# Performance work log

Hardware: AMD Instinct MI355X
Metric: run time of the kernel (lower is better)

The kernel has to match this reference:

```python
import jax, jax.numpy as jnp
import numpy as np

STEPS = 10
FIRE_RATE = 0.5
INPUT_CHANNELS = 1
EPS = 1e-5
PAD = 4  # (kernel_size-1)//2 for kernel_size=9


def setup_inputs() -> dict:
    key = jax.random.key(0)
    ks = jax.random.split(key, 8)
    B, H, W, C, HID = 4, 192, 192, 16, 128
    x = jax.random.normal(ks[0], (B, H, W, C), dtype=jnp.float32)
    rand_u = jax.random.uniform(ks[1], (STEPS, B, 1, H, W), dtype=jnp.float32)
    w_p0 = jax.random.normal(ks[2], (C, 1, 9, 9), dtype=jnp.float32) * 0.05
    b_p0 = jax.random.normal(ks[3], (C,), dtype=jnp.float32) * 0.05
    w_fc0 = jax.random.normal(ks[4], (HID, 2 * C), dtype=jnp.float32) * (1.0 / np.sqrt(2 * C))
    b_fc0 = jax.random.normal(ks[5], (HID,), dtype=jnp.float32) * 0.05
    w_fc1 = jax.random.normal(ks[6], (C, HID), dtype=jnp.float32) * (1.0 / np.sqrt(HID))
    gamma = jnp.ones((HID,), dtype=jnp.float32)
    beta = jnp.zeros((HID,), dtype=jnp.float32)
    return {"x": x, "rand_u": rand_u, "w_p0": w_p0, "b_p0": b_p0,
            "w_fc0": w_fc0, "b_fc0": b_fc0, "w_fc1": w_fc1,
            "gamma": gamma, "beta": beta}


def _depthwise(x, w, b):
    # x: [B,C,H,W], w: [C,1,9,9] depthwise, reflect padding
    xp = jnp.pad(x, ((0, 0), (0, 0), (PAD, PAD), (PAD, PAD)), mode="reflect")
    y = jax.lax.conv_general_dilated(
        xp, w, window_strides=(1, 1), padding="VALID",
        feature_group_count=x.shape[1],
        dimension_numbers=("NCHW", "OIHW", "NCHW"))
    return y + b[None, :, None, None]


def _nca_forward(x, rand_u, w_p0, b_p0, w_fc0, b_fc0, w_fc1, gamma, beta):
    x = jnp.transpose(x, (0, 3, 1, 2))  # NHWC -> NCHW

    def step(x, u):
        y1 = _depthwise(x, w_p0, b_p0)
        dx = jnp.concatenate((x, y1), axis=1)              # [B,2C,H,W]
        h = jnp.einsum("oc,bchw->bohw", w_fc0, dx) + b_fc0[None, :, None, None]
        # BatchNorm2d with track_running_stats=False: batch stats every step
        mean = jnp.mean(h, axis=(0, 2, 3), keepdims=True)
        var = jnp.mean((h - mean) ** 2, axis=(0, 2, 3), keepdims=True)
        h = gamma[None, :, None, None] * (h - mean) * jax.lax.rsqrt(var + EPS) \
            + beta[None, :, None, None]
        h = jax.nn.relu(h)
        d = jnp.einsum("oc,bchw->bohw", w_fc1, h)          # fc1, no bias
        mask = (u > FIRE_RATE).astype(x.dtype)             # [B,1,H,W]
        x2 = x + d * mask
        # keep the original input channels frozen
        x_new = jnp.concatenate((x[:, :INPUT_CHANNELS], x2[:, INPUT_CHANNELS:]), axis=1)
        return x_new, None

    x, _ = jax.lax.scan(step, x, rand_u)
    return jnp.transpose(x, (0, 2, 3, 1))  # NCHW -> NHWC


def reference(x, rand_u, w_p0, b_p0, w_fc0, b_fc0, w_fc1, gamma, beta):
    return _nca_forward(x, rand_u, w_p0, b_p0, w_fc0, b_fc0, w_fc1, gamma, beta)
```

## Files before the change

### kernel.cpp

```cpp
#include <hip/hip_runtime.h>

constexpr int Bn    = 4;
constexpr int Hn    = 192;
constexpr int Wn    = 192;
constexpr int Cn    = 16;
constexpr int HIDn  = 128;
constexpr int HWn   = Hn * Wn;
constexpr int BHWn  = Bn * HWn;
constexpr int STEPSn = 10;
constexpr int PADn  = 4;
constexpr int KSn   = 9;
constexpr float EPSf  = 1e-5f;
constexpr float FIREf = 0.5f;

constexpr int VY    = 3;
constexpr int SROWS = VY + 8;
constexpr int SCOLS = 72;
constexpr int TPXc  = 64 * VY;
constexpr int CBLK  = BHWn / TPXc;
constexpr int TPIc  = HWn / TPXc;

typedef __attribute__((ext_vector_type(8))) short short8;
typedef __attribute__((ext_vector_type(4))) float f32x4;

static __device__ __forceinline__ unsigned f2bfu(float f) {
    union { float f; unsigned u; } v; v.f = f;
    return (v.u + 0x7FFFu + ((v.u >> 16) & 1u)) >> 16;
}
static __device__ __forceinline__ short f2bf(float f) { return (short)f2bfu(f); }
static __device__ __forceinline__ float bf2f(unsigned short h) {
    union { unsigned u; float f; } v; v.u = ((unsigned)h) << 16;
    return v.f;
}
static __device__ __forceinline__ int refl(int v, int n) {
    v = v < 0 ? -v : v;
    v = v >= n ? 2 * n - 2 - v : v;
    return v;
}

__global__ void k_prep(const float* __restrict__ wp,
                       const float* __restrict__ wfc1,
                       const float* __restrict__ wfc0,
                       float* __restrict__ wtc,
                       float* __restrict__ wt1,
                       short* __restrict__ bfrag)
{
    int tid = threadIdx.x;
    for (int i = tid; i < KSn * KSn * Cn; i += 256) {
        int t = i / Cn, c = i - t * Cn;
        wtc[i] = wp[c * (KSn * KSn) + t];
    }
    for (int i = tid; i < HIDn * Cn; i += 256) {
        int o = i / Cn, c = i - o * Cn;
        wt1[i] = wfc1[c * HIDn + o];
    }
    for (int i = tid; i < 8 * 64 * 8; i += 256) {
        int nt = i >> 9;
        int rem = i & 511;
        int l = rem >> 3, j = rem & 7;
        int n = nt * 16 + (l & 15);
        int k = (l >> 4) * 8 + j;
        bfrag[i] = f2bf(wfc0[n * 32 + k]);
    }
}

#define FMA4(A, Q, V) \
    A.x = fmaf(Q.x, V.x, A.x); A.y = fmaf(Q.y, V.y, A.y); \
    A.z = fmaf(Q.z, V.z, A.z); A.w = fmaf(Q.w, V.w, A.w);

__global__ __launch_bounds__(256) void k_fused(
    const float* __restrict__ xin,
    const float* __restrict__ wtc,
    const float* __restrict__ bp,
    const short* __restrict__ bfrag,
    const float* __restrict__ bfc0,
    unsigned short* __restrict__ hbf,
    float2* __restrict__ part)
{
    __shared__ __align__(16) char smraw[4 * SROWS * SCOLS * 16];
    float4* stg = (float4*)smraw;
    float (*sdx)[33] = (float(*)[33])smraw;
    float2 (*psum)[HIDn] = (float2(*)[HIDn])(smraw + TPXc * 33 * 4);

    int tid  = threadIdx.x;
    int lane = tid & 63;
    int w    = __builtin_amdgcn_readfirstlane(tid >> 6);

    int blk = blockIdx.x;
    int b   = blk / TPIc;
    int t   = blk - b * TPIc;
    int ty  = t / 3;
    int tx  = t - ty * 3;
    int y0  = ty * VY;
    int x0  = tx * 64;

    const float4* xb4 = (const float4*)(xin + (size_t)b * HWn * Cn);
    int rrow[SROWS];
#pragma unroll
    for (int ri = 0; ri < SROWS; ++ri)
        rrow[ri] = refl(y0 + ri - PADn, Hn) * (Wn * 4);

    float4* stw = stg + w * (SROWS * SCOLS);
#pragma unroll
    for (int it = 0; it < 13; ++it) {
        int e = it * 64 + lane;
        if (e < SROWS * SCOLS) {
            int ri  = e / SCOLS;
            int col = e - ri * SCOLS;
            int gc  = refl(x0 + col - PADn, Wn);
            stw[e] = xb4[rrow[ri] + gc * 4 + w];
        }
    }

    const float4* wt4 = (const float4*)wtc;
    float4 bq = ((const float4*)bp)[w];
    float4 a0 = bq, a1 = bq, a2 = bq;
#pragma unroll
    for (int ri = 0; ri < SROWS; ++ri) {
#pragma unroll
        for (int dx = 0; dx < KSn; ++dx) {
            float4 v = stw[ri * SCOLS + lane + dx];
            if (ri <= 8)            { float4 q = wt4[(ri * KSn + dx) * 4 + w];        FMA4(a0, q, v); }
            if (ri >= 1 && ri <= 9) { float4 q = wt4[((ri - 1) * KSn + dx) * 4 + w];  FMA4(a1, q, v); }
            if (ri >= 2)            { float4 q = wt4[((ri - 2) * KSn + dx) * 4 + w];  FMA4(a2, q, v); }
        }
    }
    float4 cen0 = stw[4 * SCOLS + lane + 4];
    float4 cen1 = stw[5 * SCOLS + lane + 4];
    float4 cen2 = stw[6 * SCOLS + lane + 4];

    __syncthreads();

#pragma unroll
    for (int r = 0; r < VY; ++r) {
        int px = r * 64 + lane;
        float4 cv = r == 0 ? cen0 : (r == 1 ? cen1 : cen2);
        float4 av = r == 0 ? a0   : (r == 1 ? a1   : a2);
        sdx[px][4 * w + 0] = cv.x;  sdx[px][4 * w + 1] = cv.y;
        sdx[px][4 * w + 2] = cv.z;  sdx[px][4 * w + 3] = cv.w;
        sdx[px][Cn + 4 * w + 0] = av.x;  sdx[px][Cn + 4 * w + 1] = av.y;
        sdx[px][Cn + 4 * w + 2] = av.z;  sdx[px][Cn + 4 * w + 3] = av.w;
    }
    __syncthreads();

    int l15 = lane & 15;
    int kg  = lane >> 4;

    short8 A[3];
#pragma unroll
    for (int mt = 0; mt < 3; ++mt) {
        int px = 48 * w + mt * 16 + l15;
#pragma unroll
        for (int j = 0; j < 8; ++j)
            A[mt][j] = f2bf(sdx[px][kg * 8 + j]);
    }

    short8 Bf[8];
    const short8* bgp = (const short8*)bfrag;
#pragma unroll
    for (int nt = 0; nt < 8; ++nt) Bf[nt] = bgp[nt * 64 + lane];

#pragma unroll
    for (int nt = 0; nt < 8; ++nt) {
        int o = nt * 16 + l15;
        float bn = bfc0[o];
        float s = 0.f, q = 0.f;
#pragma unroll
        for (int mt = 0; mt < 3; ++mt) {
            f32x4 c = {bn, bn, bn, bn};
            c = __builtin_amdgcn_mfma_f32_16x16x32_bf16(A[mt], Bf[nt], c, 0, 0, 0);
            s += c[0] + c[1] + c[2] + c[3];
            q += c[0]*c[0] + c[1]*c[1] + c[2]*c[2] + c[3]*c[3];
            unsigned lo = (f2bfu(c[1]) << 16) | f2bfu(c[0]);
            unsigned hi = (f2bfu(c[3]) << 16) | f2bfu(c[2]);
            int pxb = 48 * w + 16 * mt + 4 * kg;
            int p   = (y0 + (pxb >> 6)) * Wn + x0 + (pxb & 63);
            *(uint2*)(hbf + (size_t)(b * HIDn + o) * HWn + p) = make_uint2(lo, hi);
        }
        s += __shfl_xor(s, 16, 64);  q += __shfl_xor(q, 16, 64);
        s += __shfl_xor(s, 32, 64);  q += __shfl_xor(q, 32, 64);
        if (kg == 0) psum[w][o] = make_float2(s, q);
    }
    __syncthreads();

    if (tid < HIDn) {
        float2 p0 = psum[0][tid], p1 = psum[1][tid];
        float2 p2 = psum[2][tid], p3 = psum[3][tid];
        part[(size_t)tid * CBLK + blk] =
            make_float2(p0.x + p1.x + p2.x + p3.x, p0.y + p1.y + p2.y + p3.y);
    }
}

__global__ __launch_bounds__(256) void k_combine(
    const float2* __restrict__ part,
    const float* __restrict__ gamma,
    const float* __restrict__ beta,
    float2* __restrict__ scsh)
{
    int o   = blockIdx.x;
    int tid = threadIdx.x;
    float s = 0.f, q = 0.f;
    for (int i = tid; i < CBLK; i += 256) {
        float2 v = part[(size_t)o * CBLK + i];
        s += v.x; q += v.y;
    }
#pragma unroll
    for (int off = 32; off > 0; off >>= 1) {
        s += __shfl_xor(s, off, 64);
        q += __shfl_xor(q, off, 64);
    }
    __shared__ float rs[4], rq[4];
    int wv = tid >> 6;
    if ((tid & 63) == 0) { rs[wv] = s; rq[wv] = q; }
    __syncthreads();
    if (tid == 0) {
        float S = rs[0] + rs[1] + rs[2] + rs[3];
        float Q = rq[0] + rq[1] + rq[2] + rq[3];
        float mean = S * (1.0f / BHWn);
        float var  = Q * (1.0f / BHWn) - mean * mean;
        float g    = gamma[o] * rsqrtf(var + EPSf);
        scsh[o] = make_float2(g, beta[o] - mean * g);
    }
}

__global__ __launch_bounds__(256) void k_update(
    const float* __restrict__ xin,
    const unsigned short* __restrict__ hbf,
    const float2* __restrict__ scsh,
    const float* __restrict__ wt1,
    const float* __restrict__ u,
    float* __restrict__ xout)
{
    __shared__ float pacc[4][64][17];

    int tid  = threadIdx.x;
    int lane = tid & 63;
    int w    = __builtin_amdgcn_readfirstlane(tid >> 6);

    int blk = blockIdx.x;
    int b   = blk / (HWn / 64);
    int pb  = (blk - b * (HWn / 64)) * 64;
    int p   = pb + lane;

    const unsigned short* hsrc = hbf + (size_t)b * HIDn * HWn + p;

    float acc[Cn];
#pragma unroll
    for (int c = 0; c < Cn; ++c) acc[c] = 0.f;

#pragma unroll 4
    for (int j = 0; j < 32; ++j) {
        int o = w * 32 + j;
        float2 g = scsh[o];
        float hv = bf2f(hsrc[(size_t)o * HWn]);
        float hn = fmaxf(fmaf(hv, g.x, g.y), 0.f);
        const float* wr = wt1 + o * Cn;
#pragma unroll
        for (int c = 0; c < Cn; ++c) acc[c] = fmaf(wr[c], hn, acc[c]);
    }

#pragma unroll
    for (int c = 0; c < Cn; ++c) pacc[w][lane][c] = acc[c];
    __syncthreads();

    float4 r = make_float4(0.f, 0.f, 0.f, 0.f);
#pragma unroll
    for (int w2 = 0; w2 < 4; ++w2) {
        r.x += pacc[w2][lane][4 * w + 0];
        r.y += pacc[w2][lane][4 * w + 1];
        r.z += pacc[w2][lane][4 * w + 2];
        r.w += pacc[w2][lane][4 * w + 3];
    }
    if (w == 0) r.x = 0.f;

    float m = u[(size_t)b * HWn + p] > FIREf ? 1.f : 0.f;
    size_t xoff = ((size_t)b * HWn + p) * Cn + 4 * w;
    float4 xv = *(const float4*)(xin + xoff);
    xv.x = fmaf(r.x, m, xv.x);
    xv.y = fmaf(r.y, m, xv.y);
    xv.z = fmaf(r.z, m, xv.z);
    xv.w = fmaf(r.w, m, xv.w);
    *(float4*)(xout + xoff) = xv;
}

extern "C" void kernel_launch(void* const* d_in, const int* in_sizes, int n_in,
                              void* d_out, int out_size, void* d_ws, size_t ws_size,
                              hipStream_t stream) {
    const float* x0   = (const float*)d_in[0];
    const float* ru   = (const float*)d_in[1];
    const float* wp   = (const float*)d_in[2];
    const float* bp   = (const float*)d_in[3];
    const float* wfc0 = (const float*)d_in[4];
    const float* bfc0 = (const float*)d_in[5];
    const float* wfc1 = (const float*)d_in[6];
    const float* gm   = (const float*)d_in[7];
    const float* bt   = (const float*)d_in[8];

    float* ws = (float*)d_ws;
    unsigned short* hbf = (unsigned short*)ws;
    float* xbuf  = ws + 9437184;
    float* wtc   = xbuf + 2359296;
    float* wt1   = wtc + 1312;
    short* bfrag = (short*)(wt1 + 2048);
    float2* part = (float2*)(wt1 + 2048 + 2048);
    float2* scsh = part + (size_t)HIDn * CBLK;

    k_prep<<<1, 256, 0, stream>>>(wp, wfc1, wfc0, wtc, wt1, bfrag);

    const float* xcur = x0;
    for (int s = 0; s < STEPSn; ++s) {
        k_fused<<<CBLK, 256, 0, stream>>>(xcur, wtc, bp, bfrag, bfc0, hbf, part);
        k_combine<<<HIDn, 256, 0, stream>>>(part, gm, bt, scsh);
        float* xo = (s == STEPSn - 1) ? (float*)d_out : xbuf;
        k_update<<<BHWn / 64, 256, 0, stream>>>(xcur, hbf, scsh, wt1,
                                                ru + (size_t)s * BHWn, xo);
        xcur = xo;
    }
}
```

Measured before the change: 448.5 us.

## Use MFMA for fc1, store hidden pixel-major, bf16 staging of conv input

The update kernel now computes fc1 with bf16 MFMA over a pixel-major hidden buffer instead of scalar FMAs over a channel-major one. The fused kernel writes the hidden activations in pixel-major layout, transposes the fc0 MFMA operands, and stages the conv input tile in LDS as bf16. The tile height drops from 3 to 2 rows, with a launch-bounds occupancy hint. This trades extra bf16 rounding of the state and hidden activations for fewer scalar FMAs, less LDS traffic and contiguous hidden loads.

Measured after the change: 592.1 us. 1.32x slower.

```diff
diff --git a/kernel.cpp b/kernel.cpp
--- a/kernel.cpp
+++ b/kernel.cpp
@@ -13,7 +13,7 @@
 constexpr float EPSf  = 1e-5f;
 constexpr float FIREf = 0.5f;
 
-constexpr int VY    = 3;
+constexpr int VY    = 2;
 constexpr int SROWS = VY + 8;
 constexpr int SCOLS = 72;
 constexpr int TPXc  = 64 * VY;
@@ -28,9 +28,11 @@
     return (v.u + 0x7FFFu + ((v.u >> 16) & 1u)) >> 16;
 }
 static __device__ __forceinline__ short f2bf(float f) { return (short)f2bfu(f); }
-static __device__ __forceinline__ float bf2f(unsigned short h) {
-    union { unsigned u; float f; } v; v.u = ((unsigned)h) << 16;
-    return v.f;
+static __device__ __forceinline__ unsigned pk2(float a, float b) {
+    return f2bfu(a) | (f2bfu(b) << 16);
+}
+static __device__ __forceinline__ float asf(unsigned u) {
+    union { unsigned u; float f; } v; v.u = u; return v.f;
 }
 static __device__ __forceinline__ int refl(int v, int n) {
     v = v < 0 ? -v : v;
@@ -42,33 +44,29 @@
                        const float* __restrict__ wfc1,
                        const float* __restrict__ wfc0,
                        float* __restrict__ wtc,
-                       float* __restrict__ wt1,
-                       short* __restrict__ bfrag)
+                       short* __restrict__ bfrag,
+                       short* __restrict__ w1f)
 {
     int tid = threadIdx.x;
     for (int i = tid; i < KSn * KSn * Cn; i += 256) {
         int t = i / Cn, c = i - t * Cn;
         wtc[i] = wp[c * (KSn * KSn) + t];
     }
-    for (int i = tid; i < HIDn * Cn; i += 256) {
-        int o = i / Cn, c = i - o * Cn;
-        wt1[i] = wfc1[c * HIDn + o];
-    }
     for (int i = tid; i < 8 * 64 * 8; i += 256) {
         int nt = i >> 9;
         int rem = i & 511;
         int l = rem >> 3, j = rem & 7;
-        int n = nt * 16 + (l & 15);
-        int k = (l >> 4) * 8 + j;
-        bfrag[i] = f2bf(wfc0[n * 32 + k]);
-    }
-}
-
-#define FMA4(A, Q, V) \
-    A.x = fmaf(Q.x, V.x, A.x); A.y = fmaf(Q.y, V.y, A.y); \
-    A.z = fmaf(Q.z, V.z, A.z); A.w = fmaf(Q.w, V.w, A.w);
-
-__global__ __launch_bounds__(256) void k_fused(
+        bfrag[i] = f2bf(wfc0[(nt * 16 + (l & 15)) * 32 + (l >> 4) * 8 + j]);
+    }
+    for (int i = tid; i < 4 * 64 * 8; i += 256) {
+        int ks = i >> 9;
+        int rem = i & 511;
+        int l = rem >> 3, j = rem & 7;
+        w1f[i] = f2bf(wfc1[(l & 15) * HIDn + ks * 32 + (l >> 4) * 8 + j]);
+    }
+}
+
+__global__ __launch_bounds__(256, 4) void k_fused(
     const float* __restrict__ xin,
     const float* __restrict__ wtc,
     const float* __restrict__ bp,
@@ -77,10 +75,10 @@
     unsigned short* __restrict__ hbf,
     float2* __restrict__ part)
 {
-    __shared__ __align__(16) char smraw[4 * SROWS * SCOLS * 16];
-    float4* stg = (float4*)smraw;
-    float (*sdx)[33] = (float(*)[33])smraw;
-    float2 (*psum)[HIDn] = (float2(*)[HIDn])(smraw + TPXc * 33 * 4);
+    __shared__ __align__(16) char smraw[4 * SROWS * SCOLS * 8];
+    uint2* stg = (uint2*)smraw;
+    unsigned* sdx = (unsigned*)smraw;
+    float2* psum = (float2*)(smraw + TPXc * 20 * 4);
 
     int tid  = threadIdx.x;
     int lane = tid & 63;
@@ -100,92 +98,105 @@
     for (int ri = 0; ri < SROWS; ++ri)
         rrow[ri] = refl(y0 + ri - PADn, Hn) * (Wn * 4);
 
-    float4* stw = stg + w * (SROWS * SCOLS);
-#pragma unroll
-    for (int it = 0; it < 13; ++it) {
+    uint2* stw = stg + w * (SROWS * SCOLS);
+#pragma unroll
+    for (int it = 0; it < 12; ++it) {
         int e = it * 64 + lane;
         if (e < SROWS * SCOLS) {
             int ri  = e / SCOLS;
             int col = e - ri * SCOLS;
             int gc  = refl(x0 + col - PADn, Wn);
-            stw[e] = xb4[rrow[ri] + gc * 4 + w];
+            float4 v = xb4[rrow[ri] + gc * 4 + w];
+            stw[e] = make_uint2(pk2(v.x, v.y), pk2(v.z, v.w));
         }
     }
 
     const float4* wt4 = (const float4*)wtc;
     float4 bq = ((const float4*)bp)[w];
-    float4 a0 = bq, a1 = bq, a2 = bq;
+    float4 a0 = bq, a1 = bq;
+    uint2 cen0, cen1;
 #pragma unroll
     for (int ri = 0; ri < SROWS; ++ri) {
+        uint2 tv[KSn];
+#pragma unroll
+        for (int dx = 0; dx < KSn; ++dx) tv[dx] = stw[ri * SCOLS + lane + dx];
+        if (ri == 4) cen0 = tv[4];
+        if (ri == 5) cen1 = tv[4];
 #pragma unroll
         for (int dx = 0; dx < KSn; ++dx) {
-            float4 v = stw[ri * SCOLS + lane + dx];
-            if (ri <= 8)            { float4 q = wt4[(ri * KSn + dx) * 4 + w];        FMA4(a0, q, v); }
-            if (ri >= 1 && ri <= 9) { float4 q = wt4[((ri - 1) * KSn + dx) * 4 + w];  FMA4(a1, q, v); }
-            if (ri >= 2)            { float4 q = wt4[((ri - 2) * KSn + dx) * 4 + w];  FMA4(a2, q, v); }
+            float c0 = asf(tv[dx].x << 16), c1 = asf(tv[dx].x & 0xffff0000u);
+            float c2 = asf(tv[dx].y << 16), c3 = asf(tv[dx].y & 0xffff0000u);
+            if (ri <= 8) {
+                float4 q = wt4[(ri * KSn + dx) * 4 + w];
+                a0.x = fmaf(q.x, c0, a0.x); a0.y = fmaf(q.y, c1, a0.y);
+                a0.z = fmaf(q.z, c2, a0.z); a0.w = fmaf(q.w, c3, a0.w);
+            }
+            if (ri >= 1) {
+                float4 q = wt4[((ri - 1) * KSn + dx) * 4 + w];
+                a1.x = fmaf(q.x, c0, a1.x); a1.y = fmaf(q.y, c1, a1.y);
+                a1.z = fmaf(q.z, c2, a1.z); a1.w = fmaf(q.w, c3, a1.w);
+            }
         }
     }
-    float4 cen0 = stw[4 * SCOLS + lane + 4];
-    float4 cen1 = stw[5 * SCOLS + lane + 4];
-    float4 cen2 = stw[6 * SCOLS + lane + 4];
-
     __syncthreads();
 
 #pragma unroll
     for (int r = 0; r < VY; ++r) {
         int px = r * 64 + lane;
-        float4 cv = r == 0 ? cen0 : (r == 1 ? cen1 : cen2);
-        float4 av = r == 0 ? a0   : (r == 1 ? a1   : a2);
-        sdx[px][4 * w + 0] = cv.x;  sdx[px][4 * w + 1] = cv.y;
-        sdx[px][4 * w + 2] = cv.z;  sdx[px][4 * w + 3] = cv.w;
-        sdx[px][Cn + 4 * w + 0] = av.x;  sdx[px][Cn + 4 * w + 1] = av.y;
-        sdx[px][Cn + 4 * w + 2] = av.z;  sdx[px][Cn + 4 * w + 3] = av.w;
+        uint2 cv = r ? cen1 : cen0;
+        float4 av = r ? a1 : a0;
+        unsigned* row = sdx + px * 20;
+        *(uint2*)(row + 2 * w)     = cv;
+        *(uint2*)(row + 8 + 2 * w) = make_uint2(pk2(av.x, av.y), pk2(av.z, av.w));
     }
     __syncthreads();
 
     int l15 = lane & 15;
     int kg  = lane >> 4;
 
-    short8 A[3];
-#pragma unroll
-    for (int mt = 0; mt < 3; ++mt) {
-        int px = 48 * w + mt * 16 + l15;
-#pragma unroll
-        for (int j = 0; j < 8; ++j)
-            A[mt][j] = f2bf(sdx[px][kg * 8 + j]);
-    }
-
-    short8 Bf[8];
+    short8 Bd[VY];
+#pragma unroll
+    for (int mt = 0; mt < VY; ++mt) {
+        int px = 32 * w + 16 * mt + l15;
+        Bd[mt] = *(const short8*)(sdx + px * 20 + kg * 4);
+    }
+    short8 Af[8];
     const short8* bgp = (const short8*)bfrag;
 #pragma unroll
-    for (int nt = 0; nt < 8; ++nt) Bf[nt] = bgp[nt * 64 + lane];
-
+    for (int nt = 0; nt < 8; ++nt) Af[nt] = bgp[nt * 64 + lane];
+
+    unsigned short* hb = hbf + (size_t)b * HWn * HIDn;
 #pragma unroll
     for (int nt = 0; nt < 8; ++nt) {
-        int o = nt * 16 + l15;
-        float bn = bfc0[o];
-        float s = 0.f, q = 0.f;
-#pragma unroll
-        for (int mt = 0; mt < 3; ++mt) {
-            f32x4 c = {bn, bn, bn, bn};
-            c = __builtin_amdgcn_mfma_f32_16x16x32_bf16(A[mt], Bf[nt], c, 0, 0, 0);
-            s += c[0] + c[1] + c[2] + c[3];
-            q += c[0]*c[0] + c[1]*c[1] + c[2]*c[2] + c[3]*c[3];
-            unsigned lo = (f2bfu(c[1]) << 16) | f2bfu(c[0]);
-            unsigned hi = (f2bfu(c[3]) << 16) | f2bfu(c[2]);
-            int pxb = 48 * w + 16 * mt + 4 * kg;
-            int p   = (y0 + (pxb >> 6)) * Wn + x0 + (pxb & 63);
-            *(uint2*)(hbf + (size_t)(b * HIDn + o) * HWn + p) = make_uint2(lo, hi);
+        float4 bias = ((const float4*)bfc0)[nt * 4 + kg];
+        float s[4] = {0.f, 0.f, 0.f, 0.f}, q[4] = {0.f, 0.f, 0.f, 0.f};
+#pragma unroll
+        for (int mt = 0; mt < VY; ++mt) {
+            f32x4 c = {bias.x, bias.y, bias.z, bias.w};
+            c = __builtin_amdgcn_mfma_f32_16x16x32_bf16(Af[nt], Bd[mt], c, 0, 0, 0);
+#pragma unroll
+            for (int r = 0; r < 4; ++r) { s[r] += c[r]; q[r] += c[r] * c[r]; }
+            int px = 32 * w + 16 * mt + l15;
+            int p  = (y0 + (px >> 6)) * Wn + x0 + (px & 63);
+            *(uint2*)(hb + (size_t)p * HIDn + nt * 16 + kg * 4) =
+                make_uint2(pk2(c[0], c[1]), pk2(c[2], c[3]));
         }
-        s += __shfl_xor(s, 16, 64);  q += __shfl_xor(q, 16, 64);
-        s += __shfl_xor(s, 32, 64);  q += __shfl_xor(q, 32, 64);
-        if (kg == 0) psum[w][o] = make_float2(s, q);
+#pragma unroll
+        for (int r = 0; r < 4; ++r) {
+            float sv = s[r], qv = q[r];
+            sv += __shfl_xor(sv, 1, 64);  qv += __shfl_xor(qv, 1, 64);
+            sv += __shfl_xor(sv, 2, 64);  qv += __shfl_xor(qv, 2, 64);
+            sv += __shfl_xor(sv, 4, 64);  qv += __shfl_xor(qv, 4, 64);
+            sv += __shfl_xor(sv, 8, 64);  qv += __shfl_xor(qv, 8, 64);
+            if (l15 == 0)
+                psum[w * HIDn + nt * 16 + kg * 4 + r] = make_float2(sv, qv);
+        }
     }
     __syncthreads();
 
     if (tid < HIDn) {
-        float2 p0 = psum[0][tid], p1 = psum[1][tid];
-        float2 p2 = psum[2][tid], p3 = psum[3][tid];
+        float2 p0 = psum[tid], p1 = psum[HIDn + tid];
+        float2 p2 = psum[2 * HIDn + tid], p3 = psum[3 * HIDn + tid];
         part[(size_t)tid * CBLK + blk] =
             make_float2(p0.x + p1.x + p2.x + p3.x, p0.y + p1.y + p2.y + p3.y);
     }
@@ -227,60 +238,54 @@
     const float* __restrict__ xin,
     const unsigned short* __restrict__ hbf,
     const float2* __restrict__ scsh,
-    const float* __restrict__ wt1,
+    const short* __restrict__ w1f,
     const float* __restrict__ u,
     float* __restrict__ xout)
 {
-    __shared__ float pacc[4][64][17];
-
     int tid  = threadIdx.x;
     int lane = tid & 63;
     int w    = __builtin_amdgcn_readfirstlane(tid >> 6);
+    int l15  = lane & 15;
+    int kg   = lane >> 4;
 
     int blk = blockIdx.x;
     int b   = blk / (HWn / 64);
     int pb  = (blk - b * (HWn / 64)) * 64;
-    int p   = pb + lane;
-
-    const unsigned short* hsrc = hbf + (size_t)b * HIDn * HWn + p;
-
-    float acc[Cn];
-#pragma unroll
-    for (int c = 0; c < Cn; ++c) acc[c] = 0.f;
-
-#pragma unroll 4
-    for (int j = 0; j < 32; ++j) {
-        int o = w * 32 + j;
-        float2 g = scsh[o];
-        float hv = bf2f(hsrc[(size_t)o * HWn]);
-        float hn = fmaxf(fmaf(hv, g.x, g.y), 0.f);
-        const float* wr = wt1 + o * Cn;
-#pragma unroll
-        for (int c = 0; c < Cn; ++c) acc[c] = fmaf(wr[c], hn, acc[c]);
-    }
-
-#pragma unroll
-    for (int c = 0; c < Cn; ++c) pacc[w][lane][c] = acc[c];
-    __syncthreads();
-
-    float4 r = make_float4(0.f, 0.f, 0.f, 0.f);
-#pragma unroll
-    for (int w2 = 0; w2 < 4; ++w2) {
-        r.x += pacc[w2][lane][4 * w + 0];
-        r.y += pacc[w2][lane][4 * w + 1];
-        r.z += pacc[w2][lane][4 * w + 2];
-        r.w += pacc[w2][lane][4 * w + 3];
-    }
-    if (w == 0) r.x = 0.f;
-
-    float m = u[(size_t)b * HWn + p] > FIREf ? 1.f : 0.f;
-    size_t xoff = ((size_t)b * HWn + p) * Cn + 4 * w;
-    float4 xv = *(const float4*)(xin + xoff);
-    xv.x = fmaf(r.x, m, xv.x);
-    xv.y = fmaf(r.y, m, xv.y);
-    xv.z = fmaf(r.z, m, xv.z);
-    xv.w = fmaf(r.w, m, xv.w);
-    *(float4*)(xout + xoff) = xv;
+    int pxa = pb + w * 16 + l15;
+
+    const unsigned short* hp = hbf + ((size_t)b * HWn + pxa) * HIDn + kg * 8;
+    const short8* wf  = (const short8*)w1f;
+    const float4* sc4 = (const float4*)scsh;
+
+    f32x4 c = {0.f, 0.f, 0.f, 0.f};
+#pragma unroll
+    for (int ks = 0; ks < 4; ++ks) {
+        uint4 hv = *(const uint4*)(hp + ks * 32);
+        float4 gA = sc4[ks * 16 + kg * 4 + 0];
+        float4 gB = sc4[ks * 16 + kg * 4 + 1];
+        float4 gC = sc4[ks * 16 + kg * 4 + 2];
+        float4 gD = sc4[ks * 16 + kg * 4 + 3];
+        float n0 = fmaxf(fmaf(asf(hv.x << 16),         gA.x, gA.y), 0.f);
+        float n1 = fmaxf(fmaf(asf(hv.x & 0xffff0000u), gA.z, gA.w), 0.f);
+        float n2 = fmaxf(fmaf(asf(hv.y << 16),         gB.x, gB.y), 0.f);
+        float n3 = fmaxf(fmaf(asf(hv.y & 0xffff0000u), gB.z, gB.w), 0.f);
+        float n4 = fmaxf(fmaf(asf(hv.z << 16),         gC.x, gC.y), 0.f);
+        float n5 = fmaxf(fmaf(asf(hv.z & 0xffff0000u), gC.z, gC.w), 0.f);
+        float n6 = fmaxf(fmaf(asf(hv.w << 16),         gD.x, gD.y), 0.f);
+        float n7 = fmaxf(fmaf(asf(hv.w & 0xffff0000u), gD.z, gD.w), 0.f);
+        union { uint4 u4; short8 s8; } cv;
+        cv.u4 = make_uint4(pk2(n0, n1), pk2(n2, n3), pk2(n4, n5), pk2(n6, n7));
+        c = __builtin_amdgcn_mfma_f32_16x16x32_bf16(cv.s8, wf[ks * 64 + lane], c, 0, 0, 0);
+    }
+
+#pragma unroll
+    for (int r = 0; r < 4; ++r) {
+        int pxr = pb + w * 16 + kg * 4 + r;
+        float uu = u[(size_t)b * HWn + pxr];
+        float dm = (uu > FIREf && l15 != 0) ? 1.f : 0.f;
+        size_t xo = ((size_t)b * HWn + pxr) * Cn + l15;
+        xout[xo] = fmaf(c[r], dm, xin[xo]);
+    }
 }
 
 extern "C" void kernel_launch(void* const* d_in, const int* in_sizes, int n_in,
@@ -300,19 +305,19 @@
     unsigned short* hbf = (unsigned short*)ws;
     float* xbuf  = ws + 9437184;
     float* wtc   = xbuf + 2359296;
-    float* wt1   = wtc + 1312;
-    short* bfrag = (short*)(wt1 + 2048);
-    float2* part = (float2*)(wt1 + 2048 + 2048);
+    short* bfrag = (short*)(wtc + 1312);
+    short* w1f   = bfrag + 4096;
+    float2* part = (float2*)(wtc + 1312 + 2048 + 1024);
     float2* scsh = part + (size_t)HIDn * CBLK;
 
-    k_prep<<<1, 256, 0, stream>>>(wp, wfc1, wfc0, wtc, wt1, bfrag);
+    k_prep<<<1, 256, 0, stream>>>(wp, wfc1, wfc0, wtc, bfrag, w1f);
 
     const float* xcur = x0;
     for (int s = 0; s < STEPSn; ++s) {
         k_fused<<<CBLK, 256, 0, stream>>>(xcur, wtc, bp, bfrag, bfc0, hbf, part);
         k_combine<<<HIDn, 256, 0, stream>>>(part, gm, bt, scsh);
         float* xo = (s == STEPSn - 1) ? (float*)d_out : xbuf;
-        k_update<<<BHWn / 64, 256, 0, stream>>>(xcur, hbf, scsh, wt1,
+        k_update<<<BHWn / 64, 256, 0, stream>>>(xcur, hbf, scsh, w1f,
                                                 ru + (size_t)s * BHWn, xo);
         xcur = xo;
     }
```
